# Kernel optimization log

Measured on AMD Instinct MI355X. Metric: run time of the kernel, lower is better.

## Reference

```python
import jax, jax.numpy as jnp
import numpy as np

B, FDIM, T, N, TOPK = 64, 80, 400, 5, 2
EPS = 1e-5


def conv2d(x, w, stride, pad):
    return jax.lax.conv_general_dilated(
        x, w, window_strides=stride,
        padding=[(pad, pad), (pad, pad)],
        dimension_numbers=('NCHW', 'OIHW', 'NCHW'))


def bn2d(x, g, b):
    # eval-mode BatchNorm2d with running_mean=0, running_var=1
    s = g / jnp.sqrt(1.0 + EPS)
    return x * s[None, :, None, None] + b[None, :, None, None]


def gelu(x):
    return jax.nn.gelu(x, approximate=False)  # torch nn.GELU default (erf)


def setup_inputs() -> dict:
    key = jax.random.key(0)
    ks = jax.random.split(key, 12)

    def rn(k, shape, scale=0.05):
        return jax.random.normal(k, shape, dtype=jnp.float32) * scale

    return {
        'x': rn(ks[0], (B, 1, FDIM, T, N), 1.0),
        'total': rn(ks[1], (B, 1, FDIM, 5 * T), 1.0),
        'gw1': rn(ks[2], (32, 1, 5, 15)),
        'g1': jnp.ones((32,), jnp.float32), 'b1': jnp.zeros((32,), jnp.float32),
        'gw2': rn(ks[3], (64, 32, 5, 15)),
        'g2': jnp.ones((64,), jnp.float32), 'b2': jnp.zeros((64,), jnp.float32),
        'gw3': rn(ks[4], (128, 64, 5, 15)),
        'g3': jnp.ones((128,), jnp.float32), 'b3': jnp.zeros((128,), jnp.float32),
        'gw4': rn(ks[5], (256, 128, 5, 15)),
        'g4': jnp.ones((256,), jnp.float32), 'b4': jnp.zeros((256,), jnp.float32),
        'fw1': rn(ks[6], (32, 256)), 'fb1': jnp.zeros((32,), jnp.float32),
        'g1d': jnp.ones((32,), jnp.float32), 'b1d': jnp.zeros((32,), jnp.float32),
        'fw2': rn(ks[7], (5, 32)), 'fb2': jnp.zeros((5,), jnp.float32),
        'cw1': rn(ks[8], (64, 1, 7, 14)),
    }


def reference(x, total, gw1, g1, b1, gw2, g2, b2, gw3, g3, b3, gw4, g4, b4,
              fw1, fb1, g1d, b1d, fw2, fb2, cw1):
    h = gelu(bn2d(conv2d(total, gw1, (2, 4), 2), g1, b1))
    h = gelu(bn2d(conv2d(h, gw2, (2, 4), 2), g2, b2))
    h = gelu(bn2d(conv2d(h, gw3, (2, 4), 2), g3, b3))
    h = gelu(bn2d(conv2d(h, gw4, (2, 4), 2), g4, b4))
    h = h.mean(axis=(2, 3))                      # AdaptiveAvgPool2d((1,1)) + Flatten -> [B,256]
    h = gelu(h @ fw1.T + fb1)                    # Linear(256,32) + GELU
    h = h * (g1d / jnp.sqrt(1.0 + EPS)) + b1d    # eval-mode BatchNorm1d(32)
    routing_weights = h @ fw2.T + fb2            # Linear(32,5) -> [B,5]

    # ---- top-k routing ----
    probs = jax.nn.softmax(routing_weights, axis=1)
    _, sel = jax.lax.top_k(probs, TOPK)          # [B,2]
    sel = jnp.sort(sel, axis=1)
    mask = jnp.transpose(jax.nn.one_hot(sel, N, dtype=x.dtype), (0, 2, 1))  # [B,5,2]

    # ---- one-hot einsum gather + reshape + stem conv ----
    gated = jnp.einsum('bcftn,bns->bcfts', x, mask)      # [B,1,80,T,2]
    gated = gated.reshape(-1, 1, FDIM, TOPK * gated.shape[3])  # [B,1,80,2T]
    out = conv2d(gated, cw1, (2, 2), 3)                  # [B,64,40,397]
    return out, routing_weights
```

## Files before the change

kernel.cpp:

```cpp
#include <hip/hip_runtime.h>
#include <hip/hip_bf16.h>

#define DEV __device__ __forceinline__

typedef __attribute__((ext_vector_type(8))) short short8_t;
typedef __attribute__((ext_vector_type(4))) float f32x4;

DEV float gelu_erf(float x) { return 0.5f * x * (1.0f + erff(x * 0.70710678118654752440f)); }
DEV ushort f2bf(float v) { __hip_bfloat16 h = __float2bfloat16(v); return *(ushort*)&h; }

DEV int xcd_swz(int bid, int nwg) {
    int q = nwg >> 3;
    return (bid & 7) * q + (bid >> 3);
}

__global__ void prep_k(const float* __restrict__ gw1, const float* __restrict__ gw2,
                       const float* __restrict__ gw3, const float* __restrict__ gw4,
                       const float* __restrict__ cw1,
                       ushort* __restrict__ wp1, ushort* __restrict__ wp2,
                       ushort* __restrict__ wp3, ushort* __restrict__ w4p,
                       ushort* __restrict__ wp5, ushort* __restrict__ zp)
{
    int idx = blockIdx.x * blockDim.x + threadIdx.x;
    if (idx < 2457600) {
        int kp = idx % 9600, oc = idx / 9600;
        int ic = kp & 127, kc = kp >> 7;
        w4p[idx] = f2bf(gw4[((size_t)oc * 128 + ic) * 75 + kc]);
        return;
    }
    idx -= 2457600;
    if (idx < 614400) {
        int ic = idx % 64, t = idx / 64;
        int oc = t % 128, kc = t / 128;
        wp3[idx] = f2bf(gw3[((size_t)oc * 64 + ic) * 75 + kc]);
        return;
    }
    idx -= 614400;
    if (idx < 153600) {
        int ic = idx % 32, t = idx / 32;
        int oc = t % 64, kc = t / 64;
        wp2[idx] = f2bf(gw2[((size_t)oc * 32 + ic) * 75 + kc]);
        return;
    }
    idx -= 153600;
    if (idx < 8192) {
        int oc = idx >> 7, k = idx & 127;
        int kh = k >> 4, t = k & 15;
        int a = t >> 1, c = t & 1, kw = 2 * a + c - 1;
        float v = (kh < 7 && kw >= 0 && kw < 14) ? cw1[oc * 98 + kh * 14 + kw] : 0.f;
        wp5[idx] = f2bf(v);
        return;
    }
    idx -= 8192;
    if (idx < 3072) {
        int oc = idx / 96, k = idx % 96;
        int kh = k >> 4, kw = k & 15;
        float v = (kh < 5 && kw < 15) ? gw1[oc * 75 + kh * 15 + kw] : 0.f;
        wp1[idx] = f2bf(v);
        return;
    }
    idx -= 3072;
    zp[idx] = 0;
}

template <int M_BLK, int NOC, int NCH, int NWM, int NWN, int ST, bool F32IN, bool BNG>
__global__ __launch_bounds__(64 * NWM * NWN) void convmm1_k(
    const void* __restrict__ in_, const ushort* __restrict__ wp,
    const float* __restrict__ gamma, const float* __restrict__ beta,
    void* __restrict__ out_,
    int IH, int IWE, int OH, int OW, int NOWT, int PH)
{
    constexpr int NT = 64 * NWM * NWN;
    constexpr int NR = 2 * NCH;
    constexpr int SPAN = (M_BLK - 1) * ST + 16;
    constexpr int SSTR = ((SPAN + 16 + 7) & ~7) + 8;
    constexpr int STAGE_B = NR * SSTR * 2;
    constexpr int TILE_B = BNG ? (M_BLK * NOC * 2) : (NOC * M_BLK * 4);
    constexpr int SMEM_B = STAGE_B > TILE_B ? STAGE_B : TILE_B;
    constexpr int HOFF = F32IN ? 1 : 2;
    __shared__ __align__(16) char smem[SMEM_B];
    ushort* stg = (ushort*)smem;

    int bid = xcd_swz(blockIdx.x, gridDim.x);
    const int owt = bid % NOWT; bid /= NOWT;
    const int oh = bid % OH;
    const int b  = bid / OH;
    const int ow0 = owt * M_BLK;
    const int tid = threadIdx.x;
    const int w = tid >> 6, l = tid & 63;
    const int wn = w % NWN, wm = w / NWN;
    const int m_wave = wm * 32, n_wave = wn * 32;
    const int lc = l & 15, lr = l >> 4;

    if (F32IN) {
        constexpr int NG = (SPAN + 6) / 4 + 1;
        const int iwb_al = (ow0 * ST - 2) & ~3;
        const float* inf = (const float*)in_;
        for (int u = tid; u < NR * NG; u += NT) {
            int r = u / NG, gi = u - r * NG;
            int ih = oh * 2 - PH + r;
            int iw4 = iwb_al + gi * 4;
            int q = gi * 4;
            bool rowok = (unsigned)ih < (unsigned)IH;
            if (rowok && iw4 >= 0 && iw4 + 3 < IWE) {
                float4 v = *(const float4*)&inf[((size_t)b * IH + ih) * IWE + iw4];
                ushort4 h;
                h.x = f2bf(v.x); h.y = f2bf(v.y); h.z = f2bf(v.z); h.w = f2bf(v.w);
                *(ushort4*)&stg[r * SSTR + q] = h;
            } else {
#pragma unroll
                for (int j = 0; j < 4; ++j) {
                    int iw = iw4 + j;
                    float v = (rowok && (unsigned)iw < (unsigned)IWE)
                        ? inf[((size_t)b * IH + ih) * IWE + iw] : 0.f;
                    stg[r * SSTR + q + j] = f2bf(v);
                }
            }
        }
    } else {
        constexpr int SPANU = SPAN / 2;
        constexpr int NGU = (SPANU + 6) / 4 + 1;
        const int iub_al = (ow0 - 2) & ~3;
        const uint* inu = (const uint*)in_;
        for (int u = tid; u < NR * NGU; u += NT) {
            int r = u / NGU, gi = u - r * NGU;
            int ih = oh * 2 - PH + r;
            int iu4 = iub_al + gi * 4;
            bool rowok = (unsigned)ih < (unsigned)IH;
            if (rowok && iu4 >= 0 && iu4 + 3 < IWE) {
                uint4 v = *(const uint4*)&inu[((size_t)b * IH + ih) * IWE + iu4];
                *(uint4*)&stg[r * SSTR + gi * 8] = v;
            } else {
#pragma unroll
                for (int j = 0; j < 4; ++j) {
                    int iu = iu4 + j;
                    uint v = (rowok && (unsigned)iu < (unsigned)IWE)
                        ? inu[((size_t)b * IH + ih) * IWE + iu] : 0u;
                    *(uint*)&stg[r * SSTR + gi * 8 + j * 2] = v;
                }
            }
        }
    }

    short8_t bfr[NCH][2];
    {
        const ushort* wb = wp + (size_t)(n_wave + lc) * (NCH * 32) + lr * 8;
#pragma unroll
        for (int cc = 0; cc < NCH; ++cc)
#pragma unroll
            for (int nj = 0; nj < 2; ++nj)
                bfr[cc][nj] = *(const short8_t*)(wb + (size_t)nj * 16 * (NCH * 32) + cc * 32);
    }

    __syncthreads();

    f32x4 acc[2][2];
#pragma unroll
    for (int i = 0; i < 2; ++i)
#pragma unroll
        for (int j = 0; j < 2; ++j) acc[i][j] = (f32x4){0.f, 0.f, 0.f, 0.f};

#pragma unroll
    for (int cc = 0; cc < NCH; ++cc) {
        const int kh = 2 * cc + (lr >> 1);
        const uint* lrow = (const uint*)&stg[kh * SSTR];
        short8_t a[2];
#pragma unroll
        for (int mi = 0; mi < 2; ++mi) {
            const int m = m_wave + mi * 16 + lc;
            const int half = ((m * ST + (lr & 1) * 8) >> 1) + HOFF;
            union { uint u[4]; short8_t s; } av;
            av.u[0] = lrow[half];
            av.u[1] = lrow[half + 1];
            av.u[2] = lrow[half + 2];
            av.u[3] = lrow[half + 3];
            a[mi] = av.s;
        }
#pragma unroll
        for (int mi = 0; mi < 2; ++mi)
#pragma unroll
            for (int nj = 0; nj < 2; ++nj)
                acc[mi][nj] = __builtin_amdgcn_mfma_f32_16x16x32_bf16(a[mi], bfr[cc][nj], acc[mi][nj], 0, 0, 0);
    }

    __syncthreads();

    if (BNG) {
        ushort* tile = (ushort*)smem;
#pragma unroll
        for (int nj = 0; nj < 2; ++nj) {
            const int n = n_wave + nj * 16 + lc;
            const float s = gamma[n] * rsqrtf(1.0f + 1e-5f);
            const float bb = beta[n];
#pragma unroll
            for (int mi = 0; mi < 2; ++mi)
#pragma unroll
                for (int r = 0; r < 4; ++r) {
                    const int m = m_wave + mi * 16 + lr * 4 + r;
                    float y = gelu_erf(fmaf(acc[mi][nj][r], s, bb));
                    tile[m * NOC + n] = f2bf(y);
                }
        }
        __syncthreads();
        const int mv = min(M_BLK, OW - ow0);
        uint* dst = (uint*)((ushort*)out_ + (((size_t)b * OH + oh) * OW + ow0) * NOC);
        const uint* src = (const uint*)tile;
        for (int idx = tid; idx < mv * NOC / 2; idx += NT) dst[idx] = src[idx];
    } else {
        float* tile = (float*)smem;
#pragma unroll
        for (int nj = 0; nj < 2; ++nj) {
            const int n = n_wave + nj * 16 + lc;
#pragma unroll
            for (int mi = 0; mi < 2; ++mi)
#pragma unroll
                for (int r = 0; r < 4; ++r) {
                    const int m = m_wave + mi * 16 + lr * 4 + r;
                    tile[n * M_BLK + m] = acc[mi][nj][r];
                }
        }
        __syncthreads();
        const int mv = min(M_BLK, OW - ow0);
        float* outb = (float*)out_ + ((size_t)b * NOC * OH + oh) * OW + ow0;
        for (int idx = tid; idx < NOC * mv; idx += NT) {
            int oc = idx / mv, j = idx - oc * mv;
            outb[(size_t)oc * OH * OW + j] = tile[oc * M_BLK + j];
        }
    }
}

template <int M_BLK, int OC, int ICT, int NICC, int NWM, int NWN, int UNR>
__global__ __launch_bounds__(64 * NWM * NWN) void convmm_k(
    const ushort* __restrict__ in, const ushort* __restrict__ wp,
    const float* __restrict__ gamma, const float* __restrict__ beta,
    ushort* __restrict__ out,
    int IH, int IW, int OH, int OW, int NOWT)
{
    constexpr int KH = 5, KW = 15, SW = 4;
    constexpr int MI = M_BLK / (16 * NWM);
    constexpr int NJ = OC / (16 * NWN);
    constexpr int SPAN = (M_BLK - 1) * SW + KW;
    constexpr int ICB = ICT * 2;
    constexpr int NSL = ICT / 8;
    constexpr int KEYM = NSL - 1;
    constexpr int NT = 64 * NWM * NWN;
    constexpr int NUNITS = SPAN * NSL;
    constexpr int NLD = (NUNITS + NT - 1) / NT;

    __shared__ __align__(16) ushort Abuf[SPAN * ICT];

    int bid = xcd_swz(blockIdx.x, gridDim.x);
    const int owt = bid % NOWT; bid /= NOWT;
    const int oh  = bid % OH;
    const int b   = bid / OH;
    const int ow0 = owt * M_BLK;
    const int tid = threadIdx.x;
    const int w = tid >> 6, l = tid & 63;
    const int wn = w % NWN, wm = w / NWN;
    const int m_wave = wm * (16 * MI), n_wave = wn * (16 * NJ);
    const int lc = l & 15, lr = l >> 4;

    const int ih0 = oh * 2 - 2;
    const int iw0 = ow0 * SW - 2;
    const ushort* inb = in + (size_t)b * IH * IW * ICT;

    int up[NLD], usl[NLD], uoff[NLD];
    bool uv[NLD];
#pragma unroll
    for (int i = 0; i < NLD; ++i) {
        int u = tid + i * NT;
        uv[i] = u < NUNITS;
        int uu = uv[i] ? u : 0;
        up[i] = uu / NSL;
        usl[i] = uu - up[i] * NSL;
        uoff[i] = up[i] * ICB + ((usl[i] ^ ((up[i] >> 2) & KEYM)) << 4);
    }

    uint4 rg[NLD];
    auto prefetch = [&](int kh) {
        const int ih = ih0 + kh;
        const bool rowok = (unsigned)ih < (unsigned)IH;
        const ushort* src = inb + (size_t)ih * IW * ICT;
#pragma unroll
        for (int i = 0; i < NLD; ++i) {
            int iw = iw0 + up[i];
            uint4 v = {0u, 0u, 0u, 0u};
            if (rowok && uv[i] && (unsigned)iw < (unsigned)IW)
                v = *(const uint4*)(src + (size_t)iw * ICT + usl[i] * 8);
            rg[i] = v;
        }
    };
    auto writestage = [&]() {
#pragma unroll
        for (int i = 0; i < NLD; ++i)
            if (uv[i]) *(uint4*)((char*)Abuf + uoff[i]) = rg[i];
    };

    f32x4 acc[MI][NJ];
#pragma unroll
    for (int i = 0; i < MI; ++i)
#pragma unroll
        for (int j = 0; j < NJ; ++j) acc[i][j] = (f32x4){0.f, 0.f, 0.f, 0.f};

    prefetch(0);
    writestage();
    __syncthreads();

#pragma unroll 1
    for (int kh = 0; kh < KH; ++kh) {
        if (kh + 1 < KH) prefetch(kh + 1);
        const char* buf = (const char*)Abuf;
        const ushort* wkh = wp + (size_t)(kh * KW) * OC * ICT + (size_t)(n_wave + lc) * ICT + lr * 8;
#pragma unroll UNR
        for (int kw = 0; kw < KW; ++kw) {
#pragma unroll
            for (int icc = 0; icc < NICC; ++icc) {
                short8_t a[MI], bf[NJ];
#pragma unroll
                for (int mi = 0; mi < MI; ++mi) {
                    const int r = m_wave + mi * 16 + lc;
                    const int p = SW * r + kw;
                    const int sl = icc * 4 + lr;
                    a[mi] = *(const short8_t*)(buf + p * ICB + ((sl ^ ((p >> 2) & KEYM)) << 4));
                }
                const ushort* wb = wkh + (size_t)kw * OC * ICT + icc * 32;
#pragma unroll
                for (int nj = 0; nj < NJ; ++nj)
                    bf[nj] = *(const short8_t*)(wb + (size_t)nj * 16 * ICT);
#pragma unroll
                for (int mi = 0; mi < MI; ++mi)
#pragma unroll
                    for (int nj = 0; nj < NJ; ++nj)
                        acc[mi][nj] = __builtin_amdgcn_mfma_f32_16x16x32_bf16(a[mi], bf[nj], acc[mi][nj], 0, 0, 0);
            }
        }
        if (kh + 1 < KH) {
            __syncthreads();
            writestage();
            __syncthreads();
        }
    }

    ushort* outb = out + ((size_t)b * OH + oh) * OW * OC;
#pragma unroll
    for (int nj = 0; nj < NJ; ++nj) {
        const int n = n_wave + nj * 16 + lc;
        const float s = gamma[n] * rsqrtf(1.0f + 1e-5f);
        const float bb = beta[n];
#pragma unroll
        for (int mi = 0; mi < MI; ++mi) {
#pragma unroll
            for (int r = 0; r < 4; ++r) {
                const int m = m_wave + mi * 16 + lr * 4 + r;
                const int ow = ow0 + m;
                if (ow < OW) {
                    float y = gelu_erf(fmaf(acc[mi][nj][r], s, bb));
                    outb[(size_t)ow * OC + n] = f2bf(y);
                }
            }
        }
    }
}

__global__ __launch_bounds__(256) void gemm4_k(
    const ushort* __restrict__ h3, const ushort* __restrict__ Bw,
    const ushort* __restrict__ zp, float* __restrict__ part)
{
    __shared__ __align__(16) ushort Al[3][64 * 64];
    __shared__ __align__(16) ushort Bl[3][64 * 64];
    int bid = blockIdx.x;
    const int ks = bid & 3;
    const int nt = (bid >> 2) & 3;
    const int mt = bid >> 4;
    const int m0 = mt * 64, n0 = nt * 64;
    const int k0 = (ks * 150) / 4, k1 = ((ks + 1) * 150) / 4;
    const int tid = threadIdx.x;
    const int w = tid >> 6, l = tid & 63;
    const int wr = (w >> 1) * 32, wc = (w & 1) * 32;
    const int lc = l & 15, lr = l >> 4;

    int ihb[2], iwb[2], bb[2], sspo[2];
    const ushort* gbrow[2];
#pragma unroll
    for (int i = 0; i < 2; ++i) {
        int u = tid + i * 256;
        int row = u >> 3, sl = u & 7;
        int rg = m0 + row;
        int b_ = rg / 25, p = rg - b_ * 25;
        int oh = p / 5, ow = p - oh * 5;
        bb[i] = b_;
        ihb[i] = oh * 2 - 2;
        iwb[i] = ow * 4 - 2;
        sspo[i] = (sl ^ (row & 7)) * 8;
        gbrow[i] = Bw + (size_t)(n0 + row) * 9600 + sspo[i];
    }

    auto stage = [&](int kc, int buf) {
        const int kcp = kc >> 1;
        const int kh = kcp / 15, kw = kcp - kh * 15;
        const int ice = (kc & 1) * 64;
#pragma unroll
        for (int i = 0; i < 2; ++i) {
            const int ih = ihb[i] + kh, iw = iwb[i] + kw;
            const ushort* srcA = ((unsigned)ih < 10u && (unsigned)iw < 28u)
                ? h3 + ((((size_t)bb[i] * 10 + ih) * 28 + iw) << 7) + ice + sspo[i]
                : zp;
            __builtin_amdgcn_global_load_lds(srcA, &Al[buf][(tid + i * 256) * 8], 16, 0, 0);
            __builtin_amdgcn_global_load_lds(gbrow[i] + kc * 64, &Bl[buf][(tid + i * 256) * 8], 16, 0, 0);
        }
    };

    f32x4 acc[2][2];
#pragma unroll
    for (int i = 0; i < 2; ++i)
#pragma unroll
        for (int j = 0; j < 2; ++j) acc[i][j] = (f32x4){0.f, 0.f, 0.f, 0.f};

    auto compute = [&](int buf) {
        short8_t a[2][2], bq[2][2];
#pragma unroll
        for (int mi = 0; mi < 2; ++mi)
#pragma unroll
            for (int ks_ = 0; ks_ < 2; ++ks_) {
                const int row = wr + mi * 16 + lc;
                const int sl = (ks_ * 4 + lr) ^ (row & 7);
                a[mi][ks_] = *(const short8_t*)&Al[buf][row * 64 + sl * 8];
            }
#pragma unroll
        for (int nj = 0; nj < 2; ++nj)
#pragma unroll
            for (int ks_ = 0; ks_ < 2; ++ks_) {
                const int row = wc + nj * 16 + lc;
                const int sl = (ks_ * 4 + lr) ^ (row & 7);
                bq[nj][ks_] = *(const short8_t*)&Bl[buf][row * 64 + sl * 8];
            }
#pragma unroll
        for (int ks_ = 0; ks_ < 2; ++ks_)
#pragma unroll
            for (int mi = 0; mi < 2; ++mi)
#pragma unroll
                for (int nj = 0; nj < 2; ++nj)
                    acc[mi][nj] = __builtin_amdgcn_mfma_f32_16x16x32_bf16(a[mi][ks_], bq[nj][ks_], acc[mi][nj], 0, 0, 0);
    };

    stage(k0, 0); stage(k0 + 1, 1); stage(k0 + 2, 2);
    int buf = 0;
#pragma unroll 1
    for (int kc = k0; kc < k1 - 3; ++kc) {
        asm volatile("s_waitcnt vmcnt(8)" ::: "memory");
        __syncthreads();
        compute(buf);
        __syncthreads();
        stage(kc + 3, buf);
        buf = (buf == 2) ? 0 : buf + 1;
    }
    asm volatile("s_waitcnt vmcnt(8)" ::: "memory"); __syncthreads(); compute(buf); buf = (buf == 2) ? 0 : buf + 1;
    asm volatile("s_waitcnt vmcnt(4)" ::: "memory"); __syncthreads(); compute(buf); buf = (buf == 2) ? 0 : buf + 1;
    asm volatile("s_waitcnt vmcnt(0)" ::: "memory"); __syncthreads(); compute(buf);

    float* dst = part + (size_t)ks * 409600;
#pragma unroll
    for (int mi = 0; mi < 2; ++mi)
#pragma unroll
        for (int nj = 0; nj < 2; ++nj) {
            const int n = n0 + wc + 16 * nj + lc;
#pragma unroll
            for (int r = 0; r < 4; ++r) {
                const int m = m0 + wr + 16 * mi + 4 * lr + r;
                dst[(size_t)m * 256 + n] = acc[mi][nj][r];
            }
        }
}

__global__ void route_k(const float* __restrict__ part,
                        const float* __restrict__ g4, const float* __restrict__ b4,
                        const float* __restrict__ fw1, const float* __restrict__ fb1,
                        const float* __restrict__ g1d, const float* __restrict__ b1d,
                        const float* __restrict__ fw2, const float* __restrict__ fb2,
                        float* __restrict__ rw_out, int* __restrict__ sel_out)
{
    __shared__ float pooled[256];
    __shared__ float hmid[32];
    __shared__ float rwv[5];
    const int b = blockIdx.x, c = threadIdx.x;
    const float s4 = g4[c] * rsqrtf(1.0f + 1e-5f);
    const float bb4 = b4[c];
    const float* p = part + (size_t)b * 25 * 256 + c;
    float sum = 0.f;
#pragma unroll
    for (int i = 0; i < 25; ++i) {
        float v = p[i * 256] + p[409600 + i * 256] + p[819200 + i * 256] + p[1228800 + i * 256];
        sum += gelu_erf(fmaf(v, s4, bb4));
    }
    pooled[c] = sum * (1.0f / 25.0f);
    __syncthreads();
    if (c < 32) {
        float a = fb1[c];
        const float* wr = fw1 + c * 256;
        for (int i = 0; i < 256; ++i) a += pooled[i] * wr[i];
        a = gelu_erf(a);
        a = a * (g1d[c] * rsqrtf(1.0f + 1e-5f)) + b1d[c];
        hmid[c] = a;
    }
    __syncthreads();
    if (c < 5) {
        float a = fb2[c];
        const float* wr = fw2 + c * 32;
#pragma unroll
        for (int i = 0; i < 32; ++i) a += hmid[i] * wr[i];
        rwv[c] = a;
        rw_out[b * 5 + c] = a;
    }
    __syncthreads();
    if (c == 0) {
        int i1 = 0;
        for (int i = 1; i < 5; ++i) if (rwv[i] > rwv[i1]) i1 = i;
        int i2 = -1;
        for (int i = 0; i < 5; ++i) {
            if (i == i1) continue;
            if (i2 < 0 || rwv[i] > rwv[i2]) i2 = i;
        }
        sel_out[b * 2]     = i1 < i2 ? i1 : i2;
        sel_out[b * 2 + 1] = i1 < i2 ? i2 : i1;
    }
}

__global__ void gather_k(const float* __restrict__ x, const int* __restrict__ sel,
                         uint4* __restrict__ gated)
{
    const int g = blockIdx.x * blockDim.x + threadIdx.x;
    const int idx0 = g * 4;
    const int b = idx0 / 32000;
    const int s0 = sel[b * 2], s1 = sel[b * 2 + 1];
    const float* xp = x + (size_t)idx0 * 5;
    float4 v0 = *(const float4*)(xp);
    float4 v1 = *(const float4*)(xp + 4);
    float4 v2 = *(const float4*)(xp + 8);
    float4 v3 = *(const float4*)(xp + 12);
    float4 v4 = *(const float4*)(xp + 16);
    float vals[5][4];
    vals[0][0] = v0.x; vals[1][0] = v0.y; vals[2][0] = v0.z; vals[3][0] = v0.w; vals[4][0] = v1.x;
    vals[0][1] = v1.y; vals[1][1] = v1.z; vals[2][1] = v1.w; vals[3][1] = v2.x; vals[4][1] = v2.y;
    vals[0][2] = v2.z; vals[1][2] = v2.w; vals[2][2] = v3.x; vals[3][2] = v3.y; vals[4][2] = v3.z;
    vals[0][3] = v3.w; vals[1][3] = v4.x; vals[2][3] = v4.y; vals[3][3] = v4.z; vals[4][3] = v4.w;
    uint out[4];
#pragma unroll
    for (int j = 0; j < 4; ++j) {
        float lo = vals[0][j];
        lo = (s0 == 1) ? vals[1][j] : lo;
        lo = (s0 == 2) ? vals[2][j] : lo;
        lo = (s0 == 3) ? vals[3][j] : lo;
        lo = (s0 == 4) ? vals[4][j] : lo;
        float hi = vals[0][j];
        hi = (s1 == 1) ? vals[1][j] : hi;
        hi = (s1 == 2) ? vals[2][j] : hi;
        hi = (s1 == 3) ? vals[3][j] : hi;
        hi = (s1 == 4) ? vals[4][j] : hi;
        out[j] = (uint)f2bf(lo) | ((uint)f2bf(hi) << 16);
    }
    gated[g] = (uint4){out[0], out[1], out[2], out[3]};
}

extern "C" void kernel_launch(void* const* d_in, const int* in_sizes, int n_in,
                              void* d_out, int out_size, void* d_ws, size_t ws_size,
                              hipStream_t stream)
{
    const float* x     = (const float*)d_in[0];
    const float* total = (const float*)d_in[1];
    const float* gw1 = (const float*)d_in[2];
    const float* g1  = (const float*)d_in[3];
    const float* b1  = (const float*)d_in[4];
    const float* gw2 = (const float*)d_in[5];
    const float* g2  = (const float*)d_in[6];
    const float* b2  = (const float*)d_in[7];
    const float* gw3 = (const float*)d_in[8];
    const float* g3  = (const float*)d_in[9];
    const float* b3  = (const float*)d_in[10];
    const float* gw4 = (const float*)d_in[11];
    const float* g4  = (const float*)d_in[12];
    const float* b4  = (const float*)d_in[13];
    const float* fw1 = (const float*)d_in[14];
    const float* fb1 = (const float*)d_in[15];
    const float* g1d = (const float*)d_in[16];
    const float* b1d = (const float*)d_in[17];
    const float* fw2 = (const float*)d_in[18];
    const float* fb2 = (const float*)d_in[19];
    const float* cw1 = (const float*)d_in[20];

    char* ws = (char*)d_ws;
    size_t off = 0;
    auto alloc = [&](size_t bytes) { void* p = ws + off; off = (off + bytes + 255) & ~(size_t)255; return p; };
    ushort* h1n = (ushort*)alloc((size_t)40796160 * 2);
    ushort* h2n = (ushort*)alloc((size_t)9994240 * 2);
    ushort* h3n = (ushort*)alloc((size_t)2293760 * 2);
    float* part  = (float*)alloc((size_t)4 * 409600 * 4);
    int*   sel   = (int*)alloc(512);
    uint*  gated = (uint*)alloc((size_t)2048000 * 4);
    ushort* wp1 = (ushort*)alloc((size_t)3072 * 2);
    ushort* wp2 = (ushort*)alloc((size_t)153600 * 2);
    ushort* wp3 = (ushort*)alloc((size_t)614400 * 2);
    ushort* w4p = (ushort*)alloc((size_t)2457600 * 2);
    ushort* wp5 = (ushort*)alloc((size_t)8192 * 2);
    ushort* zp  = (ushort*)alloc(512);

    float* outc = (float*)d_out;
    float* rw   = outc + (size_t)65044480;

    prep_k<<<12645, 256, 0, stream>>>(gw1, gw2, gw3, gw4, cw1, wp1, wp2, wp3, w4p, wp5, zp);

    convmm1_k<128, 32, 3, 4, 1, 4, true, true><<<64 * 40 * 4, 256, 0, stream>>>(
        total, wp1, g1, b1, h1n, 80, 2000, 40, 498, 4, 2);

    convmm_k<128, 64, 32, 1, 2, 2, 5><<<64 * 20, 256, 0, stream>>>(
        h1n, wp2, g2, b2, h2n, 40, 498, 20, 122, 1);

    convmm_k<32, 128, 64, 2, 1, 4, 5><<<64 * 10, 256, 0, stream>>>(
        h2n, wp3, g3, b3, h3n, 20, 122, 10, 28, 1);

    gemm4_k<<<400, 256, 0, stream>>>(h3n, w4p, zp, part);

    route_k<<<64, 256, 0, stream>>>(part, g4, b4, fw1, fb1, g1d, b1d, fw2, fb2, rw, sel);

    gather_k<<<2000, 256, 0, stream>>>(x, sel, (uint4*)gated);

    convmm1_k<64, 64, 4, 2, 2, 2, false, false><<<64 * 40 * 7, 256, 0, stream>>>(
        gated, wp5, nullptr, nullptr, outc, 80, 400, 40, 397, 7, 3);
}
```

Baseline: 423.7 us.

## Restructure weight prep via LDS, double gemm4 split-K, retune conv wave layouts

The weight-repack kernel now gives each output channel its own block. The block stages a contiguous slice of fp32 weights in LDS and then writes the transposed bf16 layout, replacing the earlier scattered per-element gathers across more than 12k blocks. The layer-4 GEMM split-K factor goes from 4 to 8 (800 blocks), and the routing kernel sums eight partial buffers instead of four. The conv2 and conv3 template wave configurations are changed, and conv3 now launches with 128 threads. More split-K adds partial-sum traffic, and the changed wave layouts alter occupancy and per-wave work.

```diff
diff --git a/kernel.cpp b/kernel.cpp
--- a/kernel.cpp
+++ b/kernel.cpp
@@ -14,53 +14,64 @@
     return (bid & 7) * q + (bid >> 3);
 }
 
-__global__ void prep_k(const float* __restrict__ gw1, const float* __restrict__ gw2,
-                       const float* __restrict__ gw3, const float* __restrict__ gw4,
-                       const float* __restrict__ cw1,
-                       ushort* __restrict__ wp1, ushort* __restrict__ wp2,
-                       ushort* __restrict__ wp3, ushort* __restrict__ w4p,
-                       ushort* __restrict__ wp5, ushort* __restrict__ zp)
+__global__ __launch_bounds__(256) void prep_k(
+    const float* __restrict__ gw1, const float* __restrict__ gw2,
+    const float* __restrict__ gw3, const float* __restrict__ gw4,
+    const float* __restrict__ cw1,
+    ushort* __restrict__ wp1, ushort* __restrict__ wp2,
+    ushort* __restrict__ wp3, ushort* __restrict__ w4p,
+    ushort* __restrict__ wp5, ushort* __restrict__ zp)
 {
-    int idx = blockIdx.x * blockDim.x + threadIdx.x;
-    if (idx < 2457600) {
-        int kp = idx % 9600, oc = idx / 9600;
-        int ic = kp & 127, kc = kp >> 7;
-        w4p[idx] = f2bf(gw4[((size_t)oc * 128 + ic) * 75 + kc]);
+    __shared__ float lds[9600];
+    const int tid = threadIdx.x;
+    int blk = blockIdx.x;
+    if (blk < 256) {
+        const float* src = gw4 + (size_t)blk * 9600;
+        for (int i = tid; i < 9600; i += 256) lds[i] = src[i];
+        __syncthreads();
+        ushort* dst = w4p + (size_t)blk * 9600;
+        for (int p = tid; p < 9600; p += 256) {
+            int ic = p & 127, kc = p >> 7;
+            dst[p] = f2bf(lds[ic * 75 + kc]);
+        }
         return;
     }
-    idx -= 2457600;
-    if (idx < 614400) {
-        int ic = idx % 64, t = idx / 64;
-        int oc = t % 128, kc = t / 128;
-        wp3[idx] = f2bf(gw3[((size_t)oc * 64 + ic) * 75 + kc]);
+    blk -= 256;
+    if (blk < 128) {
+        const float* src = gw3 + (size_t)blk * 4800;
+        for (int i = tid; i < 4800; i += 256) lds[i] = src[i];
+        __syncthreads();
+        for (int p = tid; p < 4800; p += 256) {
+            int ic = p & 63, kc = p >> 6;
+            wp3[(size_t)kc * 8192 + blk * 64 + ic] = f2bf(lds[ic * 75 + kc]);
+        }
         return;
     }
-    idx -= 614400;
-    if (idx < 153600) {
-        int ic = idx % 32, t = idx / 32;
-        int oc = t % 64, kc = t / 64;
-        wp2[idx] = f2bf(gw2[((size_t)oc * 32 + ic) * 75 + kc]);
+    blk -= 128;
+    if (blk < 64) {
+        const float* src = gw2 + (size_t)blk * 2400;
+        for (int i = tid; i < 2400; i += 256) lds[i] = src[i];
+        __syncthreads();
+        for (int p = tid; p < 2400; p += 256) {
+            int ic = p & 31, kc = p >> 5;
+            wp2[(size_t)kc * 2048 + blk * 32 + ic] = f2bf(lds[ic * 75 + kc]);
+        }
         return;
     }
-    idx -= 153600;
-    if (idx < 8192) {
+    for (int idx = tid; idx < 3072; idx += 256) {
+        int oc = idx / 96, k = idx % 96;
+        int kh = k >> 4, kw = k & 15;
+        float v = (kh < 5 && kw < 15) ? gw1[oc * 75 + kh * 15 + kw] : 0.f;
+        wp1[idx] = f2bf(v);
+    }
+    for (int idx = tid; idx < 8192; idx += 256) {
         int oc = idx >> 7, k = idx & 127;
         int kh = k >> 4, t = k & 15;
         int a = t >> 1, c = t & 1, kw = 2 * a + c - 1;
         float v = (kh < 7 && kw >= 0 && kw < 14) ? cw1[oc * 98 + kh * 14 + kw] : 0.f;
         wp5[idx] = f2bf(v);
-        return;
-    }
-    idx -= 8192;
-    if (idx < 3072) {
-        int oc = idx / 96, k = idx % 96;
-        int kh = k >> 4, kw = k & 15;
-        float v = (kh < 5 && kw < 15) ? gw1[oc * 75 + kh * 15 + kw] : 0.f;
-        wp1[idx] = f2bf(v);
-        return;
-    }
-    idx -= 3072;
-    zp[idx] = 0;
+    }
+    for (int idx = tid; idx < 256; idx += 256) zp[idx] = 0;
 }
 
 template <int M_BLK, int NOC, int NCH, int NWM, int NWN, int ST, bool F32IN, bool BNG>
@@ -369,11 +380,11 @@
     __shared__ __align__(16) ushort Al[3][64 * 64];
     __shared__ __align__(16) ushort Bl[3][64 * 64];
     int bid = blockIdx.x;
-    const int ks = bid & 3;
-    const int nt = (bid >> 2) & 3;
-    const int mt = bid >> 4;
+    const int ks = bid & 7;
+    const int nt = (bid >> 3) & 3;
+    const int mt = bid >> 5;
     const int m0 = mt * 64, n0 = nt * 64;
-    const int k0 = (ks * 150) / 4, k1 = ((ks + 1) * 150) / 4;
+    const int k0 = (ks * 150) / 8, k1 = ((ks + 1) * 150) / 8;
     const int tid = threadIdx.x;
     const int w = tid >> 6, l = tid & 63;
     const int wr = (w >> 1) * 32, wc = (w & 1) * 32;
@@ -489,7 +500,9 @@
     float sum = 0.f;
 #pragma unroll
     for (int i = 0; i < 25; ++i) {
-        float v = p[i * 256] + p[409600 + i * 256] + p[819200 + i * 256] + p[1228800 + i * 256];
+        float v = 0.f;
+#pragma unroll
+        for (int j = 0; j < 8; ++j) v += p[i * 256 + j * 409600];
         sum += gelu_erf(fmaf(v, s4, bb4));
     }
     pooled[c] = sum * (1.0f / 25.0f);
@@ -593,7 +606,7 @@
     ushort* h1n = (ushort*)alloc((size_t)40796160 * 2);
     ushort* h2n = (ushort*)alloc((size_t)9994240 * 2);
     ushort* h3n = (ushort*)alloc((size_t)2293760 * 2);
-    float* part  = (float*)alloc((size_t)4 * 409600 * 4);
+    float* part  = (float*)alloc((size_t)8 * 409600 * 4);
     int*   sel   = (int*)alloc(512);
     uint*  gated = (uint*)alloc((size_t)2048000 * 4);
     ushort* wp1 = (ushort*)alloc((size_t)3072 * 2);
@@ -606,18 +619,18 @@
     float* outc = (float*)d_out;
     float* rw   = outc + (size_t)65044480;
 
-    prep_k<<<12645, 256, 0, stream>>>(gw1, gw2, gw3, gw4, cw1, wp1, wp2, wp3, w4p, wp5, zp);
+    prep_k<<<449, 256, 0, stream>>>(gw1, gw2, gw3, gw4, cw1, wp1, wp2, wp3, w4p, wp5, zp);
 
     convmm1_k<128, 32, 3, 4, 1, 4, true, true><<<64 * 40 * 4, 256, 0, stream>>>(
         total, wp1, g1, b1, h1n, 80, 2000, 40, 498, 4, 2);
 
-    convmm_k<128, 64, 32, 1, 2, 2, 5><<<64 * 20, 256, 0, stream>>>(
+    convmm_k<128, 64, 32, 1, 4, 1, 5><<<64 * 20, 256, 0, stream>>>(
         h1n, wp2, g2, b2, h2n, 40, 498, 20, 122, 1);
 
-    convmm_k<32, 128, 64, 2, 1, 4, 5><<<64 * 10, 256, 0, stream>>>(
+    convmm_k<32, 128, 64, 2, 1, 2, 5><<<64 * 10, 128, 0, stream>>>(
         h2n, wp3, g3, b3, h3n, 20, 122, 10, 28, 1);
 
-    gemm4_k<<<400, 256, 0, stream>>>(h3n, w4p, zp, part);
+    gemm4_k<<<800, 256, 0, stream>>>(h3n, w4p, zp, part);
 
     route_k<<<64, 256, 0, stream>>>(part, g4, b4, fw1, fb1, g1d, b1d, fw2, fb2, rw, sel);
 
```

Result: slower. 502.3 us (+18.5%).
